# Optimization experiments

Measured on AMD Instinct MI355X. Metric: run time of the kernel, lower is better.

## Reference

```python
import jax, jax.numpy as jnp
import numpy as np

B, N, DIM = 256, 196, 384
H, KD, VD = 12, 32, 32
RES = 14
EPS = 1e-5


def _build_bias_idxs():
    pts = [(i, j) for i in range(RES) for j in range(RES)]
    offs, idxs = {}, []
    for p1 in pts:
        for p2 in pts:
            o = (abs(p1[0] - p2[0]), abs(p1[1] - p2[1]))
            if o not in offs:
                offs[o] = len(offs)
            idxs.append(offs[o])
    return jnp.asarray(np.array(idxs, dtype=np.int32).reshape(N, N))


def setup_inputs() -> dict:
    key = jax.random.key(0)
    ks = jax.random.split(key, 4)
    return {
        "x": jax.random.normal(ks[0], (B, N, DIM), dtype=jnp.float32),
        "norm_w": jnp.ones((DIM,), jnp.float32),
        "norm_b": jnp.zeros((DIM,), jnp.float32),
        "qkv_w": jax.random.normal(ks[1], (H * (VD + 2 * KD), DIM), jnp.float32) * 0.02,
        "qkv_b": jnp.zeros((H * (VD + 2 * KD),), jnp.float32),
        "attention_biases": jax.random.normal(ks[2], (H, RES * RES), jnp.float32) * 0.02,
        "proj_w": jax.random.normal(ks[3], (DIM, H * VD), jnp.float32) * 0.02,
        "proj_b": jnp.zeros((DIM,), jnp.float32),
        "bias_idxs": _build_bias_idxs(),
    }


def reference(x, norm_w, norm_b, qkv_w, qkv_b, attention_biases, proj_w, proj_b, bias_idxs):
    scale = KD ** -0.5
    # LayerNorm over feature dim
    mu = jnp.mean(x, axis=-1, keepdims=True)
    var = jnp.mean(jnp.square(x - mu), axis=-1, keepdims=True)
    xn = (x - mu) * jax.lax.rsqrt(var + EPS) * norm_w + norm_b
    # QKV projection: [B,N,H*(2*KD+VD)] -> [B,N,H,*]
    qkv = (jnp.einsum("bnd,fd->bnf", xn, qkv_w) + qkv_b).reshape(B, N, H, 2 * KD + VD)
    q, k, v = qkv[..., :KD], qkv[..., KD:2 * KD], qkv[..., 2 * KD:]
    # Relative-position bias gathered into [H,N,N]
    attn_bias = attention_biases[:, bias_idxs]
    # Scores [B,H,N,N] with bias, softmax, AV
    scores = jnp.einsum("bnhk,bmhk->bhnm", q * scale, k) + attn_bias
    probs = jax.nn.softmax(scores, axis=-1)
    out = jnp.einsum("bhnm,bmhv->bnhv", probs, v).reshape(B, N, H * VD)
    return jnp.einsum("bnf,df->bnd", out, proj_w) + proj_b
```

## Files before the change

kernel.cpp:

```cpp
#include <hip/hip_runtime.h>

#define B_    256
#define N_    196
#define NP_   208
#define VSTR_ 264
#define DIM_  384
#define H_    12
#define KD_   32
#define VD_   32
#define F_    1152
#define ROWS_ (B_ * N_)
#define SCALE_ 0.17677669529663687f
#define LOG2E_ 1.4426950408889634f
#define SCALE2_ (SCALE_ * LOG2E_)
#define EPS_  1e-5f

typedef __bf16 bf16_t;
typedef __bf16 bf16x2 __attribute__((ext_vector_type(2)));
typedef __bf16 bf16x4 __attribute__((ext_vector_type(4)));
typedef __bf16 bf16x8 __attribute__((ext_vector_type(8)));
typedef float  f32x4  __attribute__((ext_vector_type(4)));

__device__ __forceinline__ f32x4 mfma16(bf16x8 a, bf16x8 b, f32x4 c) {
    return __builtin_amdgcn_mfma_f32_16x16x32_bf16(a, b, c, 0, 0, 0);
}

__device__ __forceinline__ void gl2lds(const bf16_t* g, bf16_t* l) {
    __builtin_amdgcn_global_load_lds(
        (const __attribute__((address_space(1))) void*)g,
        (__attribute__((address_space(3))) void*)l, 16, 0, 0);
}

__global__ __launch_bounds__(256) void cvt_w(const float* __restrict__ src,
                                             bf16_t* __restrict__ dst) {
    const int i = (blockIdx.x * 256 + threadIdx.x) * 4;
    const float4 v = *(const float4*)(src + i);
    bf16x4 o = {(bf16_t)v.x, (bf16_t)v.y, (bf16_t)v.z, (bf16_t)v.w};
    *(bf16x4*)(dst + i) = o;
}

__global__ __launch_bounds__(256) void cvt_wq(const float* __restrict__ src,
                                              bf16_t* __restrict__ dst) {
    const int i = (blockIdx.x * 256 + threadIdx.x) * 4;
    const int c = (i / DIM_) % 96;
    const float s = (c >= KD_ && c < 2 * KD_) ? SCALE2_ : 1.f;
    const float4 v = *(const float4*)(src + i);
    bf16x4 o = {(bf16_t)(v.x * s), (bf16_t)(v.y * s),
                (bf16_t)(v.z * s), (bf16_t)(v.w * s)};
    *(bf16x4*)(dst + i) = o;
}

__global__ __launch_bounds__(256) void scale_qkvb(const float* __restrict__ b,
                                                  float* __restrict__ o) {
    const int f = blockIdx.x * 256 + threadIdx.x;
    if (f >= F_) return;
    const int c = f % 96;
    o[f] = b[f] * ((c >= KD_ && c < 2 * KD_) ? SCALE2_ : 1.f);
}

__global__ __launch_bounds__(256) void ln_kernel(const float* __restrict__ x,
                                                 const float* __restrict__ w,
                                                 const float* __restrict__ bvec,
                                                 bf16_t* __restrict__ xn) {
    const int lane = threadIdx.x & 63;
    const int row  = blockIdx.x * 4 + (threadIdx.x >> 6);
    const float* xr = x + (size_t)row * DIM_;
    const float4 a = *(const float4*)(xr + lane * 4);
    const float2 c = *(const float2*)(xr + 256 + lane * 2);
    float s  = a.x + a.y + a.z + a.w + c.x + c.y;
    float s2 = a.x*a.x + a.y*a.y + a.z*a.z + a.w*a.w + c.x*c.x + c.y*c.y;
    #pragma unroll
    for (int o = 32; o > 0; o >>= 1) {
        s  += __shfl_xor(s, o);
        s2 += __shfl_xor(s2, o);
    }
    const float mu = s * (1.f / 384.f);
    const float rs = rsqrtf(s2 * (1.f / 384.f) - mu * mu + EPS_);
    const float4 w4 = *(const float4*)(w + lane * 4);
    const float2 w2 = *(const float2*)(w + 256 + lane * 2);
    const float4 b4 = *(const float4*)(bvec + lane * 4);
    const float2 b2 = *(const float2*)(bvec + 256 + lane * 2);
    bf16_t* orow = xn + (size_t)row * DIM_;
    bf16x4 o4 = {(bf16_t)((a.x - mu) * rs * w4.x + b4.x),
                 (bf16_t)((a.y - mu) * rs * w4.y + b4.y),
                 (bf16_t)((a.z - mu) * rs * w4.z + b4.z),
                 (bf16_t)((a.w - mu) * rs * w4.w + b4.w)};
    *(bf16x4*)(orow + lane * 4) = o4;
    bf16x2 o2 = {(bf16_t)((c.x - mu) * rs * w2.x + b2.x),
                 (bf16_t)((c.y - mu) * rs * w2.y + b2.y)};
    *(bf16x2*)(orow + 256 + lane * 2) = o2;
}

__global__ __launch_bounds__(256) void bias_gather(const float* __restrict__ biases,
                                                   const int* __restrict__ idxs,
                                                   float* __restrict__ biasF) {
    const int e = blockIdx.x * 256 + threadIdx.x;
    if (e >= H_ * NP_ * NP_) return;
    const int h = e / (NP_ * NP_);
    const int r = e % (NP_ * NP_);
    const int m = r / NP_;
    const int q = r % NP_;
    const float v = (m < N_ && q < N_)
        ? biases[h * N_ + idxs[q * N_ + m]] * LOG2E_ : -3e30f;
    biasF[e] = v;
}

template <typename OutT>
__global__ __launch_bounds__(256) void gemm_mfma(const bf16_t* __restrict__ A,
                                                 const bf16_t* __restrict__ Wt,
                                                 const float* __restrict__ bias,
                                                 OutT* __restrict__ C,
                                                 int M, int Nout, int K) {
    __shared__ __align__(16) bf16_t As[2][128][32];
    __shared__ __align__(16) bf16_t Bs[2][128][32];
    const int tid  = threadIdx.x;
    const int lane = tid & 63;
    const int wv   = tid >> 6;
    const int ln   = lane & 15;
    const int ko   = lane >> 4;
    const int wr   = (wv >> 1) * 64;
    const int wc   = (wv & 1) * 64;

    const int NBlk   = Nout >> 7;
    const int mchunk = (M >> 7) >> 3;
    const int xcd    = blockIdx.x & 7;
    const int pos    = blockIdx.x >> 3;
    const int l_m    = xcd * mchunk + pos / NBlk;
    const int l_n    = pos % NBlk;
    const size_t bm  = (size_t)l_m * 128;
    const size_t bn  = (size_t)l_n * 128;

    const int lrow  = lane >> 2;
    const int lslot = (lane & 3) ^ ((lrow >> 1) & 3);
    const bf16_t* gA = A  + (bm + wv * 32 + lrow) * K + lslot * 8;
    const bf16_t* gB = Wt + (bn + wv * 32 + lrow) * K + lslot * 8;
    const int ldst = (wv * 32) * 32 + lane * 8;

    f32x4 acc[4][4];
    #pragma unroll
    for (int i = 0; i < 4; i++)
        #pragma unroll
        for (int j = 0; j < 4; j++)
            acc[i][j] = (f32x4){0.f, 0.f, 0.f, 0.f};

    bf16_t* As0 = &As[0][0][0];
    bf16_t* Bs0 = &Bs[0][0][0];

    #pragma unroll
    for (int c = 0; c < 2; c++) {
        gl2lds(gA + (size_t)c * 16 * K, As0 + ldst + c * 512);
        gl2lds(gB + (size_t)c * 16 * K, Bs0 + ldst + c * 512);
    }

    const int rslot = (ko ^ ((ln >> 1) & 3)) * 8;
    const int ntiles = K >> 5;
    int cur = 0;
    for (int t = 0; t < ntiles; ++t) {
        if (t + 1 < ntiles) {
            const int k0 = (t + 1) << 5;
            bf16_t* dA = As0 + (cur ^ 1) * 4096 + ldst;
            bf16_t* dB = Bs0 + (cur ^ 1) * 4096 + ldst;
            #pragma unroll
            for (int c = 0; c < 2; c++) {
                gl2lds(gA + k0 + (size_t)c * 16 * K, dA + c * 512);
                gl2lds(gB + k0 + (size_t)c * 16 * K, dB + c * 512);
            }
            asm volatile("s_waitcnt vmcnt(4)" ::: "memory");
        } else {
            asm volatile("s_waitcnt vmcnt(0)" ::: "memory");
        }
        __builtin_amdgcn_s_barrier();
        {
            bf16x8 af[4], bfr[4];
            #pragma unroll
            for (int i = 0; i < 4; i++)
                af[i] = *(const bf16x8*)&As[cur][wr + i * 16 + ln][rslot];
            #pragma unroll
            for (int j = 0; j < 4; j++)
                bfr[j] = *(const bf16x8*)&Bs[cur][wc + j * 16 + ln][rslot];
            #pragma unroll
            for (int i = 0; i < 4; i++)
                #pragma unroll
                for (int j = 0; j < 4; j++)
                    acc[i][j] = mfma16(bfr[j], af[i], acc[i][j]);
        }
        __builtin_amdgcn_s_barrier();
        cur ^= 1;
    }

    #pragma unroll
    for (int j = 0; j < 4; j++) {
        const int jc = wc + j * 16 + ko * 4;
        const float4 b4 = *(const float4*)(bias + bn + jc);
        #pragma unroll
        for (int i = 0; i < 4; i++) {
            const size_t row = bm + wr + i * 16 + ln;
            const float v0 = acc[i][j][0] + b4.x;
            const float v1 = acc[i][j][1] + b4.y;
            const float v2 = acc[i][j][2] + b4.z;
            const float v3 = acc[i][j][3] + b4.w;
            OutT* dst = C + row * (size_t)Nout + bn + jc;
            if constexpr (sizeof(OutT) == 2) {
                bf16x4 o = {(bf16_t)v0, (bf16_t)v1, (bf16_t)v2, (bf16_t)v3};
                *(bf16x4*)dst = o;
            } else {
                float4 o = {v0, v1, v2, v3};
                *(float4*)dst = o;
            }
        }
    }
}

__global__ __launch_bounds__(256) void attn_mfma(const bf16_t* __restrict__ qkv,
                                                 const float* __restrict__ biasF,
                                                 bf16_t* __restrict__ out) {
    const int b = blockIdx.x / H_;
    const int h = blockIdx.x % H_;
    __shared__ __align__(16) bf16_t Ks[NP_][32];
    __shared__ __align__(16) bf16_t Vt[VD_][VSTR_];
    const int tid  = threadIdx.x;
    const int lane = tid & 63;
    const int wv   = tid >> 6;
    const int ln   = lane & 15;
    const int ko   = lane >> 4;

    {
        const int rsub = lane >> 2;
        const int col  = (lane & 3) * 8;
        for (int c = wv; c < 13; c += 4) {
            const int row  = c * 16 + rsub;
            const int srow = min(row, N_ - 1);
            gl2lds(qkv + ((size_t)(b * N_ + srow) * H_ + h) * 96 + KD_ + col,
                   &Ks[row][col]);
        }
    }
    if (tid < 224) {
        const int m  = tid;
        const int kk = (m & ~31) + ((m & 15) >> 2) * 8 + ((m >> 4) & 1) * 4 + (m & 3);
        const bf16_t* src = qkv + ((size_t)(b * N_ + min(m, N_ - 1)) * H_ + h) * 96 + 2 * KD_;
        #pragma unroll
        for (int c4 = 0; c4 < 4; c4++) {
            bf16x8 v8 = {bf16_t(0), bf16_t(0), bf16_t(0), bf16_t(0),
                         bf16_t(0), bf16_t(0), bf16_t(0), bf16_t(0)};
            if (m < N_) v8 = *(const bf16x8*)(src + c4 * 8);
            #pragma unroll
            for (int j = 0; j < 8; j++) Vt[c4 * 8 + j][kk] = v8[j];
        }
    }
    __syncthreads();

    bf16x8 kf[13];
    #pragma unroll
    for (int c = 0; c < 13; c++)
        kf[c] = *(const bf16x8*)&Ks[c * 16 + ln][ko * 8];

    for (int t = wv; t < 13; t += 4) {
        const int q    = t * 16 + ln;
        const int qrow = min(q, N_ - 1);
        const bf16x8 qf =
            *(const bf16x8*)(qkv + ((size_t)(b * N_ + qrow) * H_ + h) * 96 + ko * 8);
        const float* bh = biasF + (size_t)h * NP_ * NP_
                        + (size_t)(ko * 4) * NP_ + t * 16 + ln;
        f32x4 sc[13];
        #pragma unroll
        for (int c = 0; c < 13; c++) {
            f32x4 z;
            #pragma unroll
            for (int r = 0; r < 4; r++) z[r] = bh[(c * 16 + r) * NP_];
            sc[c] = z;
        }
        __builtin_amdgcn_s_setprio(1);
        #pragma unroll
        for (int c = 0; c < 13; c++)
            sc[c] = mfma16(kf[c], qf, sc[c]);
        __builtin_amdgcn_s_setprio(0);

        float sum = 0.f;
        #pragma unroll
        for (int c = 0; c < 13; c++)
            #pragma unroll
            for (int r = 0; r < 4; r++) {
                const float p = exp2f(sc[c][r]);
                sc[c][r] = p;
                sum += p;
            }
        sum += __shfl_xor(sum, 16);
        sum += __shfl_xor(sum, 32);
        const float inv = 1.f / sum;

        f32x4 o0 = {0.f, 0.f, 0.f, 0.f};
        f32x4 o1 = {0.f, 0.f, 0.f, 0.f};
        __builtin_amdgcn_s_setprio(1);
        #pragma unroll
        for (int g = 0; g < 7; g++) {
            bf16x8 pf;
            #pragma unroll
            for (int jj = 0; jj < 4; jj++) pf[jj] = (bf16_t)sc[2 * g][jj];
            if (g < 6) {
                #pragma unroll
                for (int jj = 0; jj < 4; jj++) pf[4 + jj] = (bf16_t)sc[2 * g + 1][jj];
            } else {
                pf[4] = bf16_t(0); pf[5] = bf16_t(0);
                pf[6] = bf16_t(0); pf[7] = bf16_t(0);
            }
            const bf16x8 v0 = *(const bf16x8*)&Vt[ln][g * 32 + ko * 8];
            const bf16x8 v1 = *(const bf16x8*)&Vt[16 + ln][g * 32 + ko * 8];
            o0 = mfma16(v0, pf, o0);
            o1 = mfma16(v1, pf, o1);
        }
        __builtin_amdgcn_s_setprio(0);

        if (q < N_) {
            bf16_t* dst = out + (size_t)(b * N_ + q) * DIM_ + h * VD_ + ko * 4;
            bf16x4 oa = {(bf16_t)(o0[0] * inv), (bf16_t)(o0[1] * inv),
                         (bf16_t)(o0[2] * inv), (bf16_t)(o0[3] * inv)};
            bf16x4 ob = {(bf16_t)(o1[0] * inv), (bf16_t)(o1[1] * inv),
                         (bf16_t)(o1[2] * inv), (bf16_t)(o1[3] * inv)};
            *(bf16x4*)dst = oa;
            *(bf16x4*)(dst + 16) = ob;
        }
    }
}

extern "C" void kernel_launch(void* const* d_in, const int* in_sizes, int n_in,
                              void* d_out, int out_size, void* d_ws, size_t ws_size,
                              hipStream_t stream) {
    const float* x        = (const float*)d_in[0];
    const float* norm_w   = (const float*)d_in[1];
    const float* norm_b   = (const float*)d_in[2];
    const float* qkv_w    = (const float*)d_in[3];
    const float* qkv_b    = (const float*)d_in[4];
    const float* att_bias = (const float*)d_in[5];
    const float* proj_w   = (const float*)d_in[6];
    const float* proj_b   = (const float*)d_in[7];
    const int*   bias_idx = (const int*)d_in[8];
    float* out = (float*)d_out;

    char* ws = (char*)d_ws;
    size_t off = 0;
    bf16_t* xn       = (bf16_t*)(ws + off); off += (size_t)ROWS_ * DIM_ * 2;
    bf16_t* qkvbuf   = (bf16_t*)(ws + off); off += (size_t)ROWS_ * F_ * 2;
    bf16_t* attn_out = (bf16_t*)(ws + off); off += (size_t)ROWS_ * DIM_ * 2;
    float*  biasF    = (float*)(ws + off);  off += (size_t)H_ * NP_ * NP_ * 4;
    bf16_t* wq_bf    = (bf16_t*)(ws + off); off += (size_t)F_ * DIM_ * 2;
    bf16_t* wp_bf    = (bf16_t*)(ws + off); off += (size_t)DIM_ * DIM_ * 2;
    float*  qkvb_s   = (float*)(ws + off);  off += (size_t)F_ * 4;

    cvt_wq<<<(F_ * DIM_) / 1024, 256, 0, stream>>>(qkv_w, wq_bf);
    cvt_w<<<(DIM_ * DIM_) / 1024, 256, 0, stream>>>(proj_w, wp_bf);
    scale_qkvb<<<(F_ + 255) / 256, 256, 0, stream>>>(qkv_b, qkvb_s);
    ln_kernel<<<ROWS_ / 4, 256, 0, stream>>>(x, norm_w, norm_b, xn);
    bias_gather<<<(H_ * NP_ * NP_ + 255) / 256, 256, 0, stream>>>(att_bias, bias_idx, biasF);
    gemm_mfma<bf16_t><<<(ROWS_ / 128) * (F_ / 128), 256, 0, stream>>>(
        xn, wq_bf, qkvb_s, qkvbuf, ROWS_, F_, DIM_);
    attn_mfma<<<B_ * H_, 256, 0, stream>>>(qkvbuf, biasF, attn_out);
    gemm_mfma<float><<<(ROWS_ / 128) * (DIM_ / 128), 256, 0, stream>>>(
        attn_out, wp_bf, proj_b, out, ROWS_, DIM_, DIM_);
}
```

Before: 343.3 us.

## Split QKV into per-head Q/K/V buffers and retile bias for vector loads

The QKV GEMM epilogue now scatters its output into separate head-major Q, K and V buffers, so the attention kernel reads contiguous 32-element rows per (batch, head) instead of strided slices of the interleaved QKV tensor. The relative-position bias is pre-laid out so each lane loads four consecutive floats as one f32x4 instead of four strided scalars. The weight conversion, bias scaling and bias gather kernels are merged into one launch, and the GEMM is templated on K and N with a fully unrolled k-loop. The scattered epilogue stores from the QKV GEMM are less coalesced, which may offset some of the gain.

```diff
diff --git a/kernel.cpp b/kernel.cpp
--- a/kernel.cpp
+++ b/kernel.cpp
@@ -31,31 +31,49 @@
         (__attribute__((address_space(3))) void*)l, 16, 0, 0);
 }
 
-__global__ __launch_bounds__(256) void cvt_w(const float* __restrict__ src,
-                                             bf16_t* __restrict__ dst) {
-    const int i = (blockIdx.x * 256 + threadIdx.x) * 4;
-    const float4 v = *(const float4*)(src + i);
-    bf16x4 o = {(bf16_t)v.x, (bf16_t)v.y, (bf16_t)v.z, (bf16_t)v.w};
-    *(bf16x4*)(dst + i) = o;
-}
-
-__global__ __launch_bounds__(256) void cvt_wq(const float* __restrict__ src,
-                                              bf16_t* __restrict__ dst) {
-    const int i = (blockIdx.x * 256 + threadIdx.x) * 4;
-    const int c = (i / DIM_) % 96;
-    const float s = (c >= KD_ && c < 2 * KD_) ? SCALE2_ : 1.f;
-    const float4 v = *(const float4*)(src + i);
-    bf16x4 o = {(bf16_t)(v.x * s), (bf16_t)(v.y * s),
-                (bf16_t)(v.z * s), (bf16_t)(v.w * s)};
-    *(bf16x4*)(dst + i) = o;
-}
-
-__global__ __launch_bounds__(256) void scale_qkvb(const float* __restrict__ b,
-                                                  float* __restrict__ o) {
-    const int f = blockIdx.x * 256 + threadIdx.x;
-    if (f >= F_) return;
-    const int c = f % 96;
-    o[f] = b[f] * ((c >= KD_ && c < 2 * KD_) ? SCALE2_ : 1.f);
+__global__ __launch_bounds__(256) void setup_all(const float* __restrict__ qkv_w,
+                                                 const float* __restrict__ proj_w,
+                                                 const float* __restrict__ qkv_b,
+                                                 const float* __restrict__ biases,
+                                                 const int* __restrict__ idxs,
+                                                 bf16_t* __restrict__ wq_bf,
+                                                 bf16_t* __restrict__ wp_bf,
+                                                 float* __restrict__ qkvb_s,
+                                                 float* __restrict__ biasF) {
+    const int blk = blockIdx.x;
+    const int tid = threadIdx.x;
+    if (blk < 432) {
+        const int i = blk * 1024 + tid * 4;
+        const int c = (i / DIM_) % 96;
+        const float s = (c >= KD_ && c < 2 * KD_) ? SCALE2_ : 1.f;
+        const float4 v = *(const float4*)(qkv_w + i);
+        bf16x4 o = {(bf16_t)(v.x * s), (bf16_t)(v.y * s),
+                    (bf16_t)(v.z * s), (bf16_t)(v.w * s)};
+        *(bf16x4*)(wq_bf + i) = o;
+    } else if (blk < 576) {
+        const int i = (blk - 432) * 1024 + tid * 4;
+        const float4 v = *(const float4*)(proj_w + i);
+        bf16x4 o = {(bf16_t)v.x, (bf16_t)v.y, (bf16_t)v.z, (bf16_t)v.w};
+        *(bf16x4*)(wp_bf + i) = o;
+    } else if (blk < 581) {
+        const int f = (blk - 576) * 256 + tid;
+        if (f < F_) {
+            const int c = f % 96;
+            qkvb_s[f] = qkv_b[f] * ((c >= KD_ && c < 2 * KD_) ? SCALE2_ : 1.f);
+        }
+    } else {
+        const int e = (blk - 581) * 256 + tid;
+        if (e < H_ * 13 * 4 * 208 * 4) {
+            const int r  = e & 3;
+            const int q  = (e >> 2) % 208;
+            const int ko = (e / 832) & 3;
+            const int c  = (e / 3328) % 13;
+            const int h  = e / 43264;
+            const int m  = c * 16 + ko * 4 + r;
+            biasF[e] = (m < N_ && q < N_)
+                ? biases[h * N_ + idxs[q * N_ + m]] * LOG2E_ : -3e30f;
+        }
+    }
 }
 
 __global__ __launch_bounds__(256) void ln_kernel(const float* __restrict__ x,
@@ -91,26 +109,15 @@
     *(bf16x2*)(orow + 256 + lane * 2) = o2;
 }
 
-__global__ __launch_bounds__(256) void bias_gather(const float* __restrict__ biases,
-                                                   const int* __restrict__ idxs,
-                                                   float* __restrict__ biasF) {
-    const int e = blockIdx.x * 256 + threadIdx.x;
-    if (e >= H_ * NP_ * NP_) return;
-    const int h = e / (NP_ * NP_);
-    const int r = e % (NP_ * NP_);
-    const int m = r / NP_;
-    const int q = r % NP_;
-    const float v = (m < N_ && q < N_)
-        ? biases[h * N_ + idxs[q * N_ + m]] * LOG2E_ : -3e30f;
-    biasF[e] = v;
-}
-
-template <typename OutT>
+template <typename OutT, int KK, int NOUT, bool QKV>
 __global__ __launch_bounds__(256) void gemm_mfma(const bf16_t* __restrict__ A,
                                                  const bf16_t* __restrict__ Wt,
                                                  const float* __restrict__ bias,
                                                  OutT* __restrict__ C,
-                                                 int M, int Nout, int K) {
+                                                 bf16_t* __restrict__ Qg,
+                                                 bf16_t* __restrict__ Kg,
+                                                 bf16_t* __restrict__ Vg,
+                                                 int M) {
     __shared__ __align__(16) bf16_t As[2][128][32];
     __shared__ __align__(16) bf16_t Bs[2][128][32];
     const int tid  = threadIdx.x;
@@ -121,7 +128,7 @@
     const int wr   = (wv >> 1) * 64;
     const int wc   = (wv & 1) * 64;
 
-    const int NBlk   = Nout >> 7;
+    const int NBlk   = NOUT >> 7;
     const int mchunk = (M >> 7) >> 3;
     const int xcd    = blockIdx.x & 7;
     const int pos    = blockIdx.x >> 3;
@@ -132,8 +139,8 @@
 
     const int lrow  = lane >> 2;
     const int lslot = (lane & 3) ^ ((lrow >> 1) & 3);
-    const bf16_t* gA = A  + (bm + wv * 32 + lrow) * K + lslot * 8;
-    const bf16_t* gB = Wt + (bn + wv * 32 + lrow) * K + lslot * 8;
+    const bf16_t* gA = A  + (bm + wv * 32 + lrow) * KK + lslot * 8;
+    const bf16_t* gB = Wt + (bn + wv * 32 + lrow) * KK + lslot * 8;
     const int ldst = (wv * 32) * 32 + lane * 8;
 
     f32x4 acc[4][4];
@@ -148,22 +155,23 @@
 
     #pragma unroll
     for (int c = 0; c < 2; c++) {
-        gl2lds(gA + (size_t)c * 16 * K, As0 + ldst + c * 512);
-        gl2lds(gB + (size_t)c * 16 * K, Bs0 + ldst + c * 512);
+        gl2lds(gA + (size_t)c * 16 * KK, As0 + ldst + c * 512);
+        gl2lds(gB + (size_t)c * 16 * KK, Bs0 + ldst + c * 512);
     }
 
     const int rslot = (ko ^ ((ln >> 1) & 3)) * 8;
-    const int ntiles = K >> 5;
-    int cur = 0;
+    constexpr int ntiles = KK >> 5;
+    #pragma unroll
     for (int t = 0; t < ntiles; ++t) {
+        const int cur = t & 1;
         if (t + 1 < ntiles) {
             const int k0 = (t + 1) << 5;
             bf16_t* dA = As0 + (cur ^ 1) * 4096 + ldst;
             bf16_t* dB = Bs0 + (cur ^ 1) * 4096 + ldst;
             #pragma unroll
             for (int c = 0; c < 2; c++) {
-                gl2lds(gA + k0 + (size_t)c * 16 * K, dA + c * 512);
-                gl2lds(gB + k0 + (size_t)c * 16 * K, dB + c * 512);
+                gl2lds(gA + k0 + (size_t)c * 16 * KK, dA + c * 512);
+                gl2lds(gB + k0 + (size_t)c * 16 * KK, dB + c * 512);
             }
             asm volatile("s_waitcnt vmcnt(4)" ::: "memory");
         } else {
@@ -185,37 +193,67 @@
                     acc[i][j] = mfma16(bfr[j], af[i], acc[i][j]);
         }
         __builtin_amdgcn_s_barrier();
-        cur ^= 1;
-    }
-
-    #pragma unroll
-    for (int j = 0; j < 4; j++) {
-        const int jc = wc + j * 16 + ko * 4;
-        const float4 b4 = *(const float4*)(bias + bn + jc);
+    }
+
+    if constexpr (QKV) {
+        unsigned bb[4], nn[4];
         #pragma unroll
         for (int i = 0; i < 4; i++) {
-            const size_t row = bm + wr + i * 16 + ln;
-            const float v0 = acc[i][j][0] + b4.x;
-            const float v1 = acc[i][j][1] + b4.y;
-            const float v2 = acc[i][j][2] + b4.z;
-            const float v3 = acc[i][j][3] + b4.w;
-            OutT* dst = C + row * (size_t)Nout + bn + jc;
-            if constexpr (sizeof(OutT) == 2) {
-                bf16x4 o = {(bf16_t)v0, (bf16_t)v1, (bf16_t)v2, (bf16_t)v3};
-                *(bf16x4*)dst = o;
-            } else {
-                float4 o = {v0, v1, v2, v3};
-                *(float4*)dst = o;
-            }
-        }
-    }
-}
-
-__global__ __launch_bounds__(256) void attn_mfma(const bf16_t* __restrict__ qkv,
+            const unsigned row = (unsigned)(bm + wr + i * 16 + ln);
+            bb[i] = row / 196u;
+            nn[i] = row - bb[i] * 196u;
+        }
+        #pragma unroll
+        for (int j = 0; j < 4; j++) {
+            const unsigned f  = (unsigned)(bn + wc + j * 16 + ko * 4);
+            const unsigned hh = f / 96u;
+            const unsigned cc = f - hh * 96u;
+            const float4 b4 = *(const float4*)(bias + f);
+            bf16_t* segb = (cc < 32u) ? Qg : (cc < 64u) ? Kg : Vg;
+            const unsigned coff = cc & 31u;
+            #pragma unroll
+            for (int i = 0; i < 4; i++) {
+                bf16x4 o = {(bf16_t)(acc[i][j][0] + b4.x),
+                            (bf16_t)(acc[i][j][1] + b4.y),
+                            (bf16_t)(acc[i][j][2] + b4.z),
+                            (bf16_t)(acc[i][j][3] + b4.w)};
+                *(bf16x4*)(segb + ((size_t)(bb[i] * 12u + hh) * 196u + nn[i]) * 32u
+                           + coff) = o;
+            }
+        }
+    } else {
+        #pragma unroll
+        for (int j = 0; j < 4; j++) {
+            const int jc = wc + j * 16 + ko * 4;
+            const float4 b4 = *(const float4*)(bias + bn + jc);
+            #pragma unroll
+            for (int i = 0; i < 4; i++) {
+                const size_t row = bm + wr + i * 16 + ln;
+                OutT* dst = C + row * (size_t)NOUT + bn + jc;
+                if constexpr (sizeof(OutT) == 2) {
+                    bf16x4 o = {(bf16_t)(acc[i][j][0] + b4.x),
+                                (bf16_t)(acc[i][j][1] + b4.y),
+                                (bf16_t)(acc[i][j][2] + b4.z),
+                                (bf16_t)(acc[i][j][3] + b4.w)};
+                    *(bf16x4*)dst = o;
+                } else {
+                    float4 o = {acc[i][j][0] + b4.x, acc[i][j][1] + b4.y,
+                                acc[i][j][2] + b4.z, acc[i][j][3] + b4.w};
+                    *(float4*)dst = o;
+                }
+            }
+        }
+    }
+}
+
+__global__ __launch_bounds__(256) void attn_mfma(const bf16_t* __restrict__ Qg,
+                                                 const bf16_t* __restrict__ Kg,
+                                                 const bf16_t* __restrict__ Vg,
                                                  const float* __restrict__ biasF,
                                                  bf16_t* __restrict__ out) {
-    const int b = blockIdx.x / H_;
-    const int h = blockIdx.x % H_;
+    const int bh = blockIdx.x;
+    const int b  = bh / H_;
+    const int h  = bh % H_;
     __shared__ __align__(16) bf16_t Ks[NP_][32];
     __shared__ __align__(16) bf16_t Vt[VD_][VSTR_];
     const int tid  = threadIdx.x;
@@ -230,14 +268,13 @@
         for (int c = wv; c < 13; c += 4) {
             const int row  = c * 16 + rsub;
             const int srow = min(row, N_ - 1);
-            gl2lds(qkv + ((size_t)(b * N_ + srow) * H_ + h) * 96 + KD_ + col,
-                   &Ks[row][col]);
+            gl2lds(Kg + ((size_t)bh * N_ + srow) * 32 + col, &Ks[row][col]);
         }
     }
     if (tid < 224) {
         const int m  = tid;
         const int kk = (m & ~31) + ((m & 15) >> 2) * 8 + ((m >> 4) & 1) * 4 + (m & 3);
-        const bf16_t* src = qkv + ((size_t)(b * N_ + min(m, N_ - 1)) * H_ + h) * 96 + 2 * KD_;
+        const bf16_t* src = Vg + ((size_t)bh * N_ + min(m, N_ - 1)) * 32;
         #pragma unroll
         for (int c4 = 0; c4 < 4; c4++) {
             bf16x8 v8 = {bf16_t(0), bf16_t(0), bf16_t(0), bf16_t(0),
@@ -257,18 +294,13 @@
     for (int t = wv; t < 13; t += 4) {
         const int q    = t * 16 + ln;
         const int qrow = min(q, N_ - 1);
-        const bf16x8 qf =
-            *(const bf16x8*)(qkv + ((size_t)(b * N_ + qrow) * H_ + h) * 96 + ko * 8);
-        const float* bh = biasF + (size_t)h * NP_ * NP_
-                        + (size_t)(ko * 4) * NP_ + t * 16 + ln;
+        const bf16x8 qf = *(const bf16x8*)(Qg + ((size_t)bh * N_ + qrow) * 32 + ko * 8);
+        const float* bq = biasF + ((((size_t)h * 13) * 4 + ko) * 208 + q) * 4;
+
         f32x4 sc[13];
         #pragma unroll
-        for (int c = 0; c < 13; c++) {
-            f32x4 z;
-            #pragma unroll
-            for (int r = 0; r < 4; r++) z[r] = bh[(c * 16 + r) * NP_];
-            sc[c] = z;
-        }
+        for (int c = 0; c < 13; c++)
+            sc[c] = *(const f32x4*)(bq + (size_t)c * 4 * 208 * 4);
         __builtin_amdgcn_s_setprio(1);
         #pragma unroll
         for (int c = 0; c < 13; c++)
@@ -339,21 +371,21 @@
     char* ws = (char*)d_ws;
     size_t off = 0;
     bf16_t* xn       = (bf16_t*)(ws + off); off += (size_t)ROWS_ * DIM_ * 2;
-    bf16_t* qkvbuf   = (bf16_t*)(ws + off); off += (size_t)ROWS_ * F_ * 2;
+    bf16_t* Qg       = (bf16_t*)(ws + off); off += (size_t)B_ * H_ * N_ * 32 * 2;
+    bf16_t* Kg       = (bf16_t*)(ws + off); off += (size_t)B_ * H_ * N_ * 32 * 2;
+    bf16_t* Vg       = (bf16_t*)(ws + off); off += (size_t)B_ * H_ * N_ * 32 * 2;
     bf16_t* attn_out = (bf16_t*)(ws + off); off += (size_t)ROWS_ * DIM_ * 2;
-    float*  biasF    = (float*)(ws + off);  off += (size_t)H_ * NP_ * NP_ * 4;
+    float*  biasF    = (float*)(ws + off);  off += (size_t)H_ * 13 * 4 * 208 * 4 * 4;
     bf16_t* wq_bf    = (bf16_t*)(ws + off); off += (size_t)F_ * DIM_ * 2;
     bf16_t* wp_bf    = (bf16_t*)(ws + off); off += (size_t)DIM_ * DIM_ * 2;
     float*  qkvb_s   = (float*)(ws + off);  off += (size_t)F_ * 4;
 
-    cvt_wq<<<(F_ * DIM_) / 1024, 256, 0, stream>>>(qkv_w, wq_bf);
-    cvt_w<<<(DIM_ * DIM_) / 1024, 256, 0, stream>>>(proj_w, wp_bf);
-    scale_qkvb<<<(F_ + 255) / 256, 256, 0, stream>>>(qkv_b, qkvb_s);
+    setup_all<<<2609, 256, 0, stream>>>(qkv_w, proj_w, qkv_b, att_bias, bias_idx,
+                                        wq_bf, wp_bf, qkvb_s, biasF);
     ln_kernel<<<ROWS_ / 4, 256, 0, stream>>>(x, norm_w, norm_b, xn);
-    bias_gather<<<(H_ * NP_ * NP_ + 255) / 256, 256, 0, stream>>>(att_bias, bias_idx, biasF);
-    gemm_mfma<bf16_t><<<(ROWS_ / 128) * (F_ / 128), 256, 0, stream>>>(
-        xn, wq_bf, qkvb_s, qkvbuf, ROWS_, F_, DIM_);
-    attn_mfma<<<B_ * H_, 256, 0, stream>>>(qkvbuf, biasF, attn_out);
-    gemm_mfma<float><<<(ROWS_ / 128) * (DIM_ / 128), 256, 0, stream>>>(
-        attn_out, wp_bf, proj_b, out, ROWS_, DIM_, DIM_);
-}
+    gemm_mfma<bf16_t, DIM_, F_, true><<<(ROWS_ / 128) * (F_ / 128), 256, 0, stream>>>(
+        xn, wq_bf, qkvb_s, (bf16_t*)nullptr, Qg, Kg, Vg, ROWS_);
+    attn_mfma<<<B_ * H_, 256, 0, stream>>>(Qg, Kg, Vg, biasF, attn_out);
+    gemm_mfma<float, DIM_, DIM_, false><<<(ROWS_ / 128) * (DIM_ / 128), 256, 0, stream>>>(
+        attn_out, wp_bf, proj_b, out, nullptr, nullptr, nullptr, ROWS_);
+}
```

Result: faster. 317.6 us (-7.5%).
